# Optimization experiments

Hardware: AMD Instinct MI355X
Metric: run time of the kernel (lower is better)

## Reference

```python
import jax, jax.numpy as jnp
import numpy as np

B, RNN, WV, VOCAB, SRC, NMEM, OOV = 64, 512, 512, 50000, 512, 512, 50


def _gru_cell(x, h, wih, whh, bih, bhh):
    # PyTorch GRU cell. x,h: (B,RNN); wih,whh: (3*RNN, RNN)
    gi = x @ wih.T + bih
    gh = h @ whh.T + bhh
    i_r, i_z, i_n = jnp.split(gi, 3, axis=-1)
    h_r, h_z, h_n = jnp.split(gh, 3, axis=-1)
    r = jax.nn.sigmoid(i_r + h_r)
    z = jax.nn.sigmoid(i_z + h_z)
    n = jnp.tanh(i_n + r * h_n)
    return (1.0 - z) * n + z * h


def _attn_general(q, K, V, mask, W):
    # q: (B,1,D), K/V: (B,N,D), mask: (B,N), W: (D,D) (torch Linear weight, out x in)
    e = jnp.einsum('bnd,ed->bne', K, W)          # W(K)
    e = e * mask[:, :, None]
    en = jnp.einsum('btd,bnd->btn', q, e)        # (B,1,N)
    en = en * mask[:, None, :]
    # masked softmax: exp * mask, renormalize
    m = mask[:, None, :]
    ex = jnp.exp(en - jnp.max(en, axis=-1, keepdims=True)) * m
    w = ex / (jnp.sum(ex, axis=-1, keepdims=True) + 1e-10)
    ctx = jnp.einsum('btn,bnd->btd', w, V)       # (B,1,D)
    return ctx, w, en


def setup_inputs() -> dict:
    key = jax.random.key(0)
    ks = jax.random.split(key, 24)
    s = 0.05
    inp = {
        'y_t_1': jax.random.randint(ks[0], (B,), 0, VOCAB),
        's_t_1': jax.random.normal(ks[1], (1, B, RNN)) * s,
        'encoder_outputs': jax.random.normal(ks[2], (B, SRC, RNN)) * s,
        'enc_padding_mask': jnp.ones((B, SRC), jnp.float32),
        'c_t_1': jax.random.normal(ks[3], (B, 1, RNN)) * s,
        'extra_zeros': jnp.zeros((B, OOV), jnp.float32),
        'enc_batch_extend_vocab': jax.random.randint(ks[4], (B, SRC), 0, VOCAB + OOV),
        'query_memory': jax.random.normal(ks[5], (B, NMEM, RNN)) * s,
        'query_mask': jnp.ones((B, NMEM), jnp.float32),
        # parameters
        'embedding': jax.random.normal(ks[6], (VOCAB, WV)) * s,
        'x_ctx_w': jax.random.normal(ks[7], (RNN, RNN + WV)) * s,
        'x_ctx_b': jnp.zeros((RNN,), jnp.float32),
        'gru_wih': jax.random.uniform(ks[8], (3 * RNN, RNN), minval=-0.1, maxval=0.1),
        'gru_whh': jax.random.uniform(ks[9], (3 * RNN, RNN), minval=-0.1, maxval=0.1),
        'gru_bih': jnp.concatenate([jnp.zeros(RNN), jnp.ones(RNN // 2), jnp.zeros(3 * RNN - RNN - RNN // 2)]).astype(jnp.float32),
        'gru_bhh': jnp.zeros((3 * RNN,), jnp.float32),
        'readq_w': jax.random.normal(ks[10], (RNN, RNN)) * s,
        'readsrc_w': jax.random.normal(ks[11], (RNN, RNN)) * s,
        'out1_w': jax.random.normal(ks[12], (RNN, 2 * RNN)) * s,
        'out1_b': jnp.zeros((RNN,), jnp.float32),
        'out2_w': jax.random.normal(ks[13], (VOCAB, RNN)) * s,
        'out2_b': jnp.zeros((VOCAB,), jnp.float32),
    }
    return inp


def reference(y_t_1, s_t_1, encoder_outputs, enc_padding_mask, c_t_1, extra_zeros,
              enc_batch_extend_vocab, query_memory, query_mask,
              embedding, x_ctx_w, x_ctx_b, gru_wih, gru_whh, gru_bih, gru_bhh,
              readq_w, readsrc_w, out1_w, out1_b, out2_w, out2_b):
    # embed current token and mix with previous context
    y_emb = embedding[y_t_1]                                   # (B,WV)
    x = jnp.concatenate([c_t_1, y_emb[:, None, :]], axis=-1)   # (B,1,RNN+WV)
    x = x @ x_ctx_w.T + x_ctx_b                                # (B,1,RNN)

    h = s_t_1[0]                                               # (B,RNN)
    h = _gru_cell(x[:, 0], h, gru_wih, gru_whh, gru_bih, gru_bhh)

    # NTM memory read + second GRU step (loop runs once in the source)
    c_mem, _, _ = _attn_general(h[:, None, :], query_memory, query_memory, query_mask, readq_w)
    h = _gru_cell(c_mem[:, 0], h, gru_wih, gru_whh, gru_bih, gru_bhh)

    # source attention
    c_t, attn_dist, _ = _attn_general(h[:, None, :], encoder_outputs, encoder_outputs, enc_padding_mask, readsrc_w)

    out = jnp.concatenate([h, c_t[:, 0]], axis=-1)             # (B,2*RNN)
    out = out @ out1_w.T + out1_b
    out = out @ out2_w.T + out2_b                              # (B,VOCAB)
    vocab_dist = jax.nn.softmax(out, axis=-1)

    vocab_dist_ = 0.5 * vocab_dist
    attn_dist_ = 0.5 * attn_dist[:, 0]                         # (B,SRC)
    vocab_dist_ = jnp.concatenate([vocab_dist_, extra_zeros], axis=-1)  # (B,VOCAB+OOV)

    # copy-mechanism scatter_add along vocab dim, per batch row
    final_dist = jax.vmap(lambda v, idx, a: v.at[idx].add(a))(
        vocab_dist_, enc_batch_extend_vocab, attn_dist_)

    s_t = h[None]                                              # (1,B,RNN)
    return final_dist, s_t, c_t, attn_dist
```

## Files before the change

### kernel.cpp

```cpp
#include <hip/hip_runtime.h>

#define BATCH 64
#define RNN   512
#define VOCAB 50000
#define OOV   50
#define VEXT  50050
#define NSRC  512
#define NOB2  391

typedef short bf16x8 __attribute__((ext_vector_type(8)));
typedef float f32x4  __attribute__((ext_vector_type(4)));

__device__ __forceinline__ float sigmoidf_(float x) { return 1.f / (1.f + __expf(-x)); }

__device__ __forceinline__ float gru_one(float ir, float iz, float inn,
                                         float hr, float hz, float hn, float h)
{
    const float r = sigmoidf_(ir + hr);
    const float z = sigmoidf_(iz + hz);
    const float n = tanhf(inn + r * hn);
    return (1.f - z) * n + z * h;
}

__device__ __forceinline__ short f2bf(float x) {
    unsigned u = __builtin_bit_cast(unsigned, x);
    unsigned r = (u + 0x7FFFu + ((u >> 16) & 1u)) >> 16;
    return (short)r;
}

template<bool WT>
__global__ __launch_bounds__(256) void k_gemm_small(
    const float* __restrict__ A0, const float* __restrict__ W0,
    const float* __restrict__ bias0, float* __restrict__ C0, int asum0,
    const float* __restrict__ A1, const float* __restrict__ W1,
    const float* __restrict__ bias1, float* __restrict__ C1, int asum1,
    int K, int O)
{
    const float* A = A0; const float* W = W0; const float* bias = bias0;
    float* C = C0; int asum = asum0;
    if (blockIdx.z == 1) { A = A1; W = W1; bias = bias1; C = C1; asum = asum1; }

    __shared__ float As[32 * 64];
    __shared__ float Ws[32 * 32];
    const int t  = threadIdx.x;
    const int tx = t & 15, ty = t >> 4;
    const int o0 = blockIdx.x * 32;
    const int kchunk = K >> 2;
    const int kbeg = blockIdx.y * kchunk;
    const int kend = kbeg + kchunk;
    float acc[4][2] = {};
    const int ab  = t >> 2;
    const int akq = (t & 3) * 4;

    for (int k0 = kbeg; k0 < kend; k0 += 32) {
        {
            const float* Ap = &A[(size_t)ab * K + k0 + akq];
            float4 v0 = *(const float4*)Ap;
            float4 v1 = *(const float4*)(Ap + 16);
            if (asum) {
                #pragma unroll
                for (int s = 1; s < 4; s++) {
                    const float* Aps = Ap + (size_t)s * 64 * K;
                    float4 w0 = *(const float4*)Aps;
                    float4 w1 = *(const float4*)(Aps + 16);
                    v0.x += w0.x; v0.y += w0.y; v0.z += w0.z; v0.w += w0.w;
                    v1.x += w1.x; v1.y += w1.y; v1.z += w1.z; v1.w += w1.w;
                }
            }
            As[(akq+0)*64+ab]=v0.x; As[(akq+1)*64+ab]=v0.y; As[(akq+2)*64+ab]=v0.z; As[(akq+3)*64+ab]=v0.w;
            As[(akq+16)*64+ab]=v1.x; As[(akq+17)*64+ab]=v1.y; As[(akq+18)*64+ab]=v1.z; As[(akq+19)*64+ab]=v1.w;
        }
        if (WT) {
            const int o  = t >> 3;
            const int kq = (t & 7) * 4;
            float4 v = *(const float4*)&W[(size_t)(o0 + o) * K + k0 + kq];
            Ws[(kq+0)*32+o]=v.x; Ws[(kq+1)*32+o]=v.y; Ws[(kq+2)*32+o]=v.z; Ws[(kq+3)*32+o]=v.w;
        } else {
            const int kk = t >> 3;
            const int oq = (t & 7) * 4;
            *(float4*)&Ws[kk*32 + oq] = *(const float4*)&W[(size_t)(k0 + kk) * O + o0 + oq];
        }
        __syncthreads();
        #pragma unroll
        for (int kk = 0; kk < 32; kk++) {
            float4 a4 = *(const float4*)&As[kk*64 + ty*4];
            float2 w2 = *(const float2*)&Ws[kk*32 + tx*2];
            acc[0][0] = fmaf(a4.x, w2.x, acc[0][0]); acc[0][1] = fmaf(a4.x, w2.y, acc[0][1]);
            acc[1][0] = fmaf(a4.y, w2.x, acc[1][0]); acc[1][1] = fmaf(a4.y, w2.y, acc[1][1]);
            acc[2][0] = fmaf(a4.z, w2.x, acc[2][0]); acc[2][1] = fmaf(a4.z, w2.y, acc[2][1]);
            acc[3][0] = fmaf(a4.w, w2.x, acc[3][0]); acc[3][1] = fmaf(a4.w, w2.y, acc[3][1]);
        }
        __syncthreads();
    }
    const int o = o0 + tx*2;
    float b0v = 0.f, b1v = 0.f;
    if (bias && blockIdx.y == 0) { b0v = bias[o]; b1v = bias[o+1]; }
    float* Cp = C + (size_t)blockIdx.y * 64 * O;
    #pragma unroll
    for (int j = 0; j < 4; j++) {
        const int bb = ty*4 + j;
        Cp[(size_t)bb*O + o]     = acc[j][0] + b0v;
        Cp[(size_t)bb*O + o + 1] = acc[j][1] + b1v;
    }
}

__global__ __launch_bounds__(256) void k_gemm_x0(
    const int* __restrict__ yidx, const float* __restrict__ ct1, const float* __restrict__ emb,
    const float* __restrict__ W, const float* __restrict__ bias, float* __restrict__ C)
{
    __shared__ float As[32 * 64];
    __shared__ float Ws[32 * 32];
    const int t  = threadIdx.x;
    const int tx = t & 15, ty = t >> 4;
    const int o0 = blockIdx.x * 32;
    const int kbeg = blockIdx.y * 256;
    const int kend = kbeg + 256;
    float acc[4][2] = {};
    const int ab  = t >> 2;
    const int akq = (t & 3) * 4;
    const int erow = yidx[ab];

    for (int k0 = kbeg; k0 < kend; k0 += 32) {
        {
            const float* src = (k0 < 512) ? (ct1 + (size_t)ab * 512 + k0)
                                          : (emb + (size_t)erow * 512 + (k0 - 512));
            float4 v0 = *(const float4*)(src + akq);
            float4 v1 = *(const float4*)(src + akq + 16);
            As[(akq+0)*64+ab]=v0.x; As[(akq+1)*64+ab]=v0.y; As[(akq+2)*64+ab]=v0.z; As[(akq+3)*64+ab]=v0.w;
            As[(akq+16)*64+ab]=v1.x; As[(akq+17)*64+ab]=v1.y; As[(akq+18)*64+ab]=v1.z; As[(akq+19)*64+ab]=v1.w;
        }
        {
            const int o  = t >> 3;
            const int kq = (t & 7) * 4;
            float4 v = *(const float4*)&W[(size_t)(o0 + o) * 1024 + k0 + kq];
            Ws[(kq+0)*32+o]=v.x; Ws[(kq+1)*32+o]=v.y; Ws[(kq+2)*32+o]=v.z; Ws[(kq+3)*32+o]=v.w;
        }
        __syncthreads();
        #pragma unroll
        for (int kk = 0; kk < 32; kk++) {
            float4 a4 = *(const float4*)&As[kk*64 + ty*4];
            float2 w2 = *(const float2*)&Ws[kk*32 + tx*2];
            acc[0][0] = fmaf(a4.x, w2.x, acc[0][0]); acc[0][1] = fmaf(a4.x, w2.y, acc[0][1]);
            acc[1][0] = fmaf(a4.y, w2.x, acc[1][0]); acc[1][1] = fmaf(a4.y, w2.y, acc[1][1]);
            acc[2][0] = fmaf(a4.z, w2.x, acc[2][0]); acc[2][1] = fmaf(a4.z, w2.y, acc[2][1]);
            acc[3][0] = fmaf(a4.w, w2.x, acc[3][0]); acc[3][1] = fmaf(a4.w, w2.y, acc[3][1]);
        }
        __syncthreads();
    }
    const int o = o0 + tx*2;
    float b0v = 0.f, b1v = 0.f;
    if (blockIdx.y == 0) { b0v = bias[o]; b1v = bias[o+1]; }
    float* Cp = C + (size_t)blockIdx.y * 64 * 512;
    #pragma unroll
    for (int j = 0; j < 4; j++) {
        const int bb = ty*4 + j;
        Cp[(size_t)bb*512 + o]     = acc[j][0] + b0v;
        Cp[(size_t)bb*512 + o + 1] = acc[j][1] + b1v;
    }
}

template<int KS>
__global__ __launch_bounds__(256) void k_gemm_gru(
    const float* __restrict__ gi, const float* __restrict__ gh,
    const float* __restrict__ hprev, const float* __restrict__ W,
    float* __restrict__ C, float* __restrict__ hout, float* __restrict__ cat_out)
{
    __shared__ float As[32 * 64];
    __shared__ float Ws[32 * 32];
    const int t  = threadIdx.x;
    const int tx = t & 15, ty = t >> 4;
    const int o0 = blockIdx.x * 32;
    const int kchunk = 512 / KS;
    const int kbeg = blockIdx.y * kchunk;
    const int kend = kbeg + kchunk;
    float acc[4][2] = {};
    const int ab  = t >> 2;
    const int akq = (t & 3) * 4;

    for (int k0 = kbeg; k0 < kend; k0 += 32) {
        #pragma unroll
        for (int half = 0; half < 2; half++) {
            const int d = k0 + akq + half * 16;
            float irv[4] = {0,0,0,0}, izv[4] = {0,0,0,0}, inv_[4] = {0,0,0,0};
            float hrv[4] = {0,0,0,0}, hzv[4] = {0,0,0,0}, hnv[4] = {0,0,0,0};
            #pragma unroll
            for (int s = 0; s < 4; s++) {
                const float* gp = gi + (size_t)s * BATCH * 1536 + (size_t)ab * 1536 + d;
                const float* hp = gh + (size_t)s * BATCH * 1536 + (size_t)ab * 1536 + d;
                float4 a0 = *(const float4*)(gp);
                float4 a1 = *(const float4*)(gp + 512);
                float4 a2 = *(const float4*)(gp + 1024);
                float4 b0 = *(const float4*)(hp);
                float4 b1 = *(const float4*)(hp + 512);
                float4 b2 = *(const float4*)(hp + 1024);
                irv[0]+=a0.x; irv[1]+=a0.y; irv[2]+=a0.z; irv[3]+=a0.w;
                izv[0]+=a1.x; izv[1]+=a1.y; izv[2]+=a1.z; izv[3]+=a1.w;
                inv_[0]+=a2.x; inv_[1]+=a2.y; inv_[2]+=a2.z; inv_[3]+=a2.w;
                hrv[0]+=b0.x; hrv[1]+=b0.y; hrv[2]+=b0.z; hrv[3]+=b0.w;
                hzv[0]+=b1.x; hzv[1]+=b1.y; hzv[2]+=b1.z; hzv[3]+=b1.w;
                hnv[0]+=b2.x; hnv[1]+=b2.y; hnv[2]+=b2.z; hnv[3]+=b2.w;
            }
            const float4 hq = *(const float4*)(hprev + (size_t)ab * 512 + d);
            float o0v = gru_one(irv[0], izv[0], inv_[0], hrv[0], hzv[0], hnv[0], hq.x);
            float o1v = gru_one(irv[1], izv[1], inv_[1], hrv[1], hzv[1], hnv[1], hq.y);
            float o2v = gru_one(irv[2], izv[2], inv_[2], hrv[2], hzv[2], hnv[2], hq.z);
            float o3v = gru_one(irv[3], izv[3], inv_[3], hrv[3], hzv[3], hnv[3], hq.w);
            const int kk = akq + half * 16;
            As[(kk+0)*64+ab] = o0v; As[(kk+1)*64+ab] = o1v;
            As[(kk+2)*64+ab] = o2v; As[(kk+3)*64+ab] = o3v;
            if (blockIdx.x == 0) {
                float4 ov = make_float4(o0v, o1v, o2v, o3v);
                *(float4*)&hout[(size_t)ab * 512 + d] = ov;
                if (cat_out) *(float4*)&cat_out[(size_t)ab * 1024 + d] = ov;
            }
        }
        {
            const int kk = t >> 3;
            const int oq = (t & 7) * 4;
            *(float4*)&Ws[kk*32 + oq] = *(const float4*)&W[(size_t)(k0 + kk) * 512 + o0 + oq];
        }
        __syncthreads();
        #pragma unroll
        for (int kk = 0; kk < 32; kk++) {
            float4 a4 = *(const float4*)&As[kk*64 + ty*4];
            float2 w2 = *(const float2*)&Ws[kk*32 + tx*2];
            acc[0][0] = fmaf(a4.x, w2.x, acc[0][0]); acc[0][1] = fmaf(a4.x, w2.y, acc[0][1]);
            acc[1][0] = fmaf(a4.y, w2.x, acc[1][0]); acc[1][1] = fmaf(a4.y, w2.y, acc[1][1]);
            acc[2][0] = fmaf(a4.z, w2.x, acc[2][0]); acc[2][1] = fmaf(a4.z, w2.y, acc[2][1]);
            acc[3][0] = fmaf(a4.w, w2.x, acc[3][0]); acc[3][1] = fmaf(a4.w, w2.y, acc[3][1]);
        }
        __syncthreads();
    }
    const int o = o0 + tx*2;
    float* Cp = C + (size_t)blockIdx.y * 64 * 512;
    #pragma unroll
    for (int j = 0; j < 4; j++) {
        const int bb = ty*4 + j;
        Cp[(size_t)bb*512 + o]     = acc[j][0];
        Cp[(size_t)bb*512 + o + 1] = acc[j][1];
    }
}

__global__ __launch_bounds__(256) void k_attn_pass(
    const float* __restrict__ KV, const float* __restrict__ Upart,
    const float* __restrict__ mask, float* __restrict__ en, float* __restrict__ part)
{
    const int b = blockIdx.y;
    const int chunk = blockIdx.x;
    const int t = threadIdx.x;
    const int lane = t & 63;
    const int wv = t >> 6;
    const float* KVb = KV + (size_t)b * NSRC * RNN;

    const int r0 = chunk * 32 + wv * 8;

    float4 x[8][2];
    float mk[8];
    #pragma unroll
    for (int i = 0; i < 8; i++) {
        const float* rp = KVb + (size_t)(r0 + i) * RNN + lane * 8;
        x[i][0] = *(const float4*)rp;
        x[i][1] = *(const float4*)(rp + 4);
    }
    #pragma unroll
    for (int i = 0; i < 8; i++) mk[i] = mask[(size_t)b * NSRC + r0 + i];

    float4 u0, u1;
    {
        const float* up = Upart + (size_t)b * RNN + lane * 8;
        u0 = *(const float4*)up; u1 = *(const float4*)(up + 4);
        #pragma unroll
        for (int s = 1; s < 8; s++) {
            const float* ups = up + (size_t)s * BATCH * RNN;
            float4 a = *(const float4*)ups; float4 c = *(const float4*)(ups + 4);
            u0.x += a.x; u0.y += a.y; u0.z += a.z; u0.w += a.w;
            u1.x += c.x; u1.y += c.y; u1.z += c.z; u1.w += c.w;
        }
    }

    float m_run = -1e30f, s_run = 0.f;
    float acc[8] = {0,0,0,0,0,0,0,0};
    #pragma unroll
    for (int i = 0; i < 8; i++) {
        const int n = r0 + i;
        float d = x[i][0].x*u0.x + x[i][0].y*u0.y + x[i][0].z*u0.z + x[i][0].w*u0.w
                + x[i][1].x*u1.x + x[i][1].y*u1.y + x[i][1].z*u1.z + x[i][1].w*u1.w;
        #pragma unroll
        for (int off = 32; off; off >>= 1) d += __shfl_xor(d, off);
        const float s = d * mk[i] * mk[i];
        if (lane == 0) en[(size_t)b * NSRC + n] = s;
        const float mnew = fmaxf(m_run, s);
        const float sc = __expf(m_run - mnew);
        const float w  = __expf(s - mnew) * mk[i];
        s_run = s_run * sc + w;
        acc[0] = acc[0]*sc + w*x[i][0].x; acc[1] = acc[1]*sc + w*x[i][0].y;
        acc[2] = acc[2]*sc + w*x[i][0].z; acc[3] = acc[3]*sc + w*x[i][0].w;
        acc[4] = acc[4]*sc + w*x[i][1].x; acc[5] = acc[5]*sc + w*x[i][1].y;
        acc[6] = acc[6]*sc + w*x[i][1].z; acc[7] = acc[7]*sc + w*x[i][1].w;
        m_run = mnew;
    }
    __shared__ float sm[4], ss[4];
    __shared__ float sacc[4][512];
    *(float4*)&sacc[wv][lane*8]     = make_float4(acc[0], acc[1], acc[2], acc[3]);
    *(float4*)&sacc[wv][lane*8 + 4] = make_float4(acc[4], acc[5], acc[6], acc[7]);
    if (lane == 0) { sm[wv] = m_run; ss[wv] = s_run; }
    __syncthreads();
    const float M = fmaxf(fmaxf(sm[0], sm[1]), fmaxf(sm[2], sm[3]));
    const float e0 = __expf(sm[0]-M), e1 = __expf(sm[1]-M), e2 = __expf(sm[2]-M), e3 = __expf(sm[3]-M);
    const float S = ss[0]*e0 + ss[1]*e1 + ss[2]*e2 + ss[3]*e3;
    float* pp = part + (size_t)(b * 16 + chunk) * 514;
    const int c = t;
    pp[2 + c]       = sacc[0][c]*e0 + sacc[1][c]*e1 + sacc[2][c]*e2 + sacc[3][c]*e3;
    pp[2 + c + 256] = sacc[0][c+256]*e0 + sacc[1][c+256]*e1 + sacc[2][c+256]*e2 + sacc[3][c+256]*e3;
    if (t == 0) { pp[0] = M; pp[1] = S; }
}

__global__ __launch_bounds__(128) void k_attn_combine(
    const float* __restrict__ part, const float* __restrict__ en,
    const float* __restrict__ mask, float* __restrict__ ctx,
    float* __restrict__ ctx2, float* __restrict__ attn_out)
{
    const int b = blockIdx.x, z = blockIdx.y, t = threadIdx.x;
    const float* pb = part + (size_t)b * 16 * 514;
    float M = -1e30f;
    #pragma unroll
    for (int c = 0; c < 16; c++) M = fmaxf(M, pb[c * 514]);
    float e[16]; float S = 0.f;
    #pragma unroll
    for (int c = 0; c < 16; c++) { e[c] = __expf(pb[c * 514] - M); S += pb[c * 514 + 1] * e[c]; }
    const float inv = 1.f / (S + 1e-10f);
    const int d = z * 128 + t;
    float a = 0.f;
    #pragma unroll
    for (int c = 0; c < 16; c++) a += pb[c * 514 + 2 + d] * e[c];
    const float val = a * inv;
    ctx[(size_t)b * 512 + d] = val;
    if (ctx2) ctx2[(size_t)b * 1024 + d] = val;
    if (attn_out)
        attn_out[(size_t)b * NSRC + d] = __expf(en[(size_t)b * NSRC + d] - M) * mask[(size_t)b * NSRC + d] * inv;
}

__global__ void k_tobf16(const float* __restrict__ in, short* __restrict__ outp)
{
    const int i = blockIdx.x * 256 + threadIdx.x;
    const float v = in[i] + in[32768 + i] + in[65536 + i] + in[98304 + i];
    outp[i] = f2bf(v);
}

__global__ __launch_bounds__(512, 4) void k_out2_mfma(
    const short* __restrict__ Abf, const float* __restrict__ W2,
    const float* __restrict__ bias, float* __restrict__ C, float* __restrict__ bstat)
{
    __shared__ alignas(16) short As[64 * 512];
    __shared__ float smax[8][64];
    __shared__ float ssum[8][64];
    const int t = threadIdx.x;
    const int lane = t & 63, wv = t >> 6;

    {
        char* Asb = (char*)As;
        const char* Ab = (const char*)Abf;
        #pragma unroll
        for (int it = 0; it < 8; ++it) {
            const int off = (it * 512 + t) * 16;
            const int row = off >> 10;
            const int kb  = off & 1023;
            bf16x8 v = *(const bf16x8*)(Ab + off);
            *(bf16x8*)(Asb + row * 1024 + (kb ^ ((row & 7) << 4))) = v;
        }
    }
    __syncthreads();

    const int l15 = lane & 15, g = lane >> 4;
    const int goff = g * 8;
    const int obase = blockIdx.x * 128 + wv * 16;
    const int ocol = obase + l15;
    const bool valid = (ocol < VOCAB);
    const int orow = valid ? ocol : (VOCAB - 1);
    const float* wr = &W2[(size_t)orow * RNN + goff];

    const int sw = (l15 & 7) << 4;
    const char* a0b = (const char*)As + (l15     ) * 1024;
    const char* a1b = (const char*)As + (l15 + 16) * 1024;
    const char* a2b = (const char*)As + (l15 + 32) * 1024;
    const char* a3b = (const char*)As + (l15 + 48) * 1024;

    f32x4 acc0 = {0,0,0,0}, acc1 = {0,0,0,0}, acc2 = {0,0,0,0}, acc3 = {0,0,0,0};

    float4 p0a = *(const float4*)(wr);
    float4 p0b = *(const float4*)(wr + 4);
    float4 p1a = *(const float4*)(wr + 32);
    float4 p1b = *(const float4*)(wr + 36);
    #pragma unroll 4
    for (int k0 = 0; k0 < RNN; k0 += 32) {
        const int kn = (k0 + 64) & 511;
        float4 n0 = *(const float4*)(wr + kn);
        float4 n1 = *(const float4*)(wr + kn + 4);
        const int kb = ((k0 + goff) * 2) ^ sw;
        bf16x8 a0 = *(const bf16x8*)(a0b + kb);
        bf16x8 a1 = *(const bf16x8*)(a1b + kb);
        bf16x8 a2 = *(const bf16x8*)(a2b + kb);
        bf16x8 a3 = *(const bf16x8*)(a3b + kb);
        bf16x8 bf;
        bf[0]=f2bf(p0a.x); bf[1]=f2bf(p0a.y); bf[2]=f2bf(p0a.z); bf[3]=f2bf(p0a.w);
        bf[4]=f2bf(p0b.x); bf[5]=f2bf(p0b.y); bf[6]=f2bf(p0b.z); bf[7]=f2bf(p0b.w);
        acc0 = __builtin_amdgcn_mfma_f32_16x16x32_bf16(a0, bf, acc0, 0, 0, 0);
        acc1 = __builtin_amdgcn_mfma_f32_16x16x32_bf16(a1, bf, acc1, 0, 0, 0);
        acc2 = __builtin_amdgcn_mfma_f32_16x16x32_bf16(a2, bf, acc2, 0, 0, 0);
        acc3 = __builtin_amdgcn_mfma_f32_16x16x32_bf16(a3, bf, acc3, 0, 0, 0);
        p0a = p1a; p0b = p1b; p1a = n0; p1b = n1;
    }

    const float bv = valid ? bias[ocol] : 0.f;
    float lv[4][4];
    #pragma unroll
    for (int r = 0; r < 4; r++) {
        lv[0][r] = valid ? acc0[r] + bv : -1e30f;
        lv[1][r] = valid ? acc1[r] + bv : -1e30f;
        lv[2][r] = valid ? acc2[r] + bv : -1e30f;
        lv[3][r] = valid ? acc3[r] + bv : -1e30f;
    }
    if (valid) {
        #pragma unroll
        for (int q = 0; q < 4; q++)
            #pragma unroll
            for (int r = 0; r < 4; r++)
                C[(size_t)(q*16 + g*4 + r) * VOCAB + ocol] = lv[q][r];
    }

    #pragma unroll
    for (int q = 0; q < 4; q++) {
        #pragma unroll
        for (int r = 0; r < 4; r++) {
            float m = lv[q][r];
            m = fmaxf(m, __shfl_xor(m, 1));
            m = fmaxf(m, __shfl_xor(m, 2));
            m = fmaxf(m, __shfl_xor(m, 4));
            m = fmaxf(m, __shfl_xor(m, 8));
            if (l15 == 0) smax[wv][q*16 + g*4 + r] = m;
        }
    }
    __syncthreads();
    if (t < 64) {
        float m = smax[0][t];
        #pragma unroll
        for (int w = 1; w < 8; w++) m = fmaxf(m, smax[w][t]);
        smax[0][t] = m;
    }
    __syncthreads();
    #pragma unroll
    for (int q = 0; q < 4; q++) {
        #pragma unroll
        for (int r = 0; r < 4; r++) {
            const int row = q*16 + g*4 + r;
            float e = __expf(lv[q][r] - smax[0][row]);
            e += __shfl_xor(e, 1);
            e += __shfl_xor(e, 2);
            e += __shfl_xor(e, 4);
            e += __shfl_xor(e, 8);
            if (l15 == 0) ssum[wv][row] = e;
        }
    }
    __syncthreads();
    if (t < 64) {
        float s = 0.f;
        #pragma unroll
        for (int w = 0; w < 8; w++) s += ssum[w][t];
        bstat[((size_t)t * NOB2 + blockIdx.x) * 2 + 0] = smax[0][t];
        bstat[((size_t)t * NOB2 + blockIdx.x) * 2 + 1] = s;
    }
}

__global__ __launch_bounds__(256) void k_statred(const float* __restrict__ bstat, float* __restrict__ stat)
{
    const int b = blockIdx.x, t = threadIdx.x;
    const float* pr = bstat + (size_t)b * NOB2 * 2;
    __shared__ float red[8];
    float m = -1e30f;
    for (int i = t; i < NOB2; i += 256) m = fmaxf(m, pr[i*2]);
    #pragma unroll
    for (int off = 32; off; off >>= 1) m = fmaxf(m, __shfl_xor(m, off));
    if ((t & 63) == 0) red[t >> 6] = m;
    __syncthreads();
    m = fmaxf(fmaxf(red[0], red[1]), fmaxf(red[2], red[3]));
    __syncthreads();
    float s = 0.f;
    for (int i = t; i < NOB2; i += 256) s += pr[i*2+1] * __expf(pr[i*2] - m);
    #pragma unroll
    for (int off = 32; off; off >>= 1) s += __shfl_xor(s, off);
    if ((t & 63) == 0) red[(t >> 6) + 4] = s;
    __syncthreads();
    if (t == 0) { stat[b*2] = m; stat[b*2+1] = red[4]+red[5]+red[6]+red[7]; }
}

__global__ void k_final(const float* __restrict__ L, const float* __restrict__ stat,
                        const float* __restrict__ ez, float* __restrict__ out)
{
    const int b = blockIdx.y;
    const int v = blockIdx.x * 256 + threadIdx.x;
    if (v >= VEXT) return;
    const float M = stat[b * 2];
    const float inv = 0.5f / stat[b * 2 + 1];
    float r;
    if (v < VOCAB) r = __expf(L[(size_t)b * VOCAB + v] - M) * inv;
    else           r = ez[(size_t)b * OOV + (v - VOCAB)];
    out[(size_t)b * VEXT + v] = r;
}

__global__ void k_scatter(const int* __restrict__ idx, const float* __restrict__ attn,
                          float* __restrict__ out)
{
    const int b = blockIdx.x, j = threadIdx.x;
    const int v = idx[(size_t)b * NSRC + j];
    atomicAdd(&out[(size_t)b * VEXT + v], 0.5f * attn[(size_t)b * NSRC + j]);
}

extern "C" void kernel_launch(void* const* d_in, const int* in_sizes, int n_in,
                              void* d_out, int out_size, void* d_ws, size_t ws_size,
                              hipStream_t stream)
{
    (void)in_sizes; (void)n_in; (void)out_size; (void)ws_size;
    const int*   y     = (const int*)  d_in[0];
    const float* st1   = (const float*)d_in[1];
    const float* enc   = (const float*)d_in[2];
    const float* encM  = (const float*)d_in[3];
    const float* ct1   = (const float*)d_in[4];
    const float* ez    = (const float*)d_in[5];
    const int*   ebev  = (const int*)  d_in[6];
    const float* qmem  = (const float*)d_in[7];
    const float* qmask = (const float*)d_in[8];
    const float* emb   = (const float*)d_in[9];
    const float* xw    = (const float*)d_in[10];
    const float* xb    = (const float*)d_in[11];
    const float* wih   = (const float*)d_in[12];
    const float* whh   = (const float*)d_in[13];
    const float* bih   = (const float*)d_in[14];
    const float* bhh   = (const float*)d_in[15];
    const float* rqw   = (const float*)d_in[16];
    const float* rsw   = (const float*)d_in[17];
    const float* o1w   = (const float*)d_in[18];
    const float* o1b   = (const float*)d_in[19];
    const float* o2w   = (const float*)d_in[20];
    const float* o2b   = (const float*)d_in[21];

    float* ws  = (float*)d_ws;
    float* out = (float*)d_out;

    constexpr size_t WS_PART = 0;
    constexpr size_t WS_EN   = 526336;
    constexpr size_t WS_H1   = 559104;
    constexpr size_t WS_CTX1 = 591872;
    constexpr size_t WS_LOG  = 0;
    constexpr size_t WS_GIP  = 3200000;
    constexpr size_t WS_GHP  = 3593216;
    constexpr size_t WS_UP   = 3986432;
    constexpr size_t WS_XP   = 3986432;
    constexpr size_t WS_O1P  = 3986432;
    constexpr size_t WS_ABF  = 4117504;
    constexpr size_t WS_CAT2 = 4248576;
    constexpr size_t WS_BSTAT= 4314112;
    constexpr size_t WS_STAT = 4364160;

    constexpr size_t OUT_ST = 3203200, OUT_CT = 3235968, OUT_ATTN = 3268736;

    float* part = ws + WS_PART;
    float* en   = ws + WS_EN;
    float* h1   = ws + WS_H1;
    float* ctx1 = ws + WS_CTX1;
    float* logi = ws + WS_LOG;
    float* gip  = ws + WS_GIP;
    float* ghp  = ws + WS_GHP;
    float* up   = ws + WS_UP;
    float* xp   = ws + WS_XP;
    float* o1p  = ws + WS_O1P;
    float* cat2 = ws + WS_CAT2;
    float* bstat= ws + WS_BSTAT;
    float* stat = ws + WS_STAT;
    short* abf  = (short*)(ws + WS_ABF);

    k_gemm_x0<<<dim3(16,4), 256, 0, stream>>>(y, ct1, emb, xw, xb, xp);
    k_gemm_small<true><<<dim3(48,4,2), 256, 0, stream>>>(xp, wih, bih, gip, 1,
                                                         st1, whh, bhh, ghp, 0, 512, 1536);
    k_gemm_gru<8><<<dim3(16,8), 256, 0, stream>>>(gip, ghp, st1, rqw, up, h1, nullptr);
    k_attn_pass<<<dim3(16,64), 256, 0, stream>>>(qmem, up, qmask, en, part);
    k_attn_combine<<<dim3(64,4), 128, 0, stream>>>(part, en, qmask, ctx1, nullptr, nullptr);
    k_gemm_small<true><<<dim3(48,4,2), 256, 0, stream>>>(ctx1, wih, bih, gip, 0,
                                                         h1, whh, bhh, ghp, 0, 512, 1536);
    k_gemm_gru<8><<<dim3(16,8), 256, 0, stream>>>(gip, ghp, h1, rsw, up, out + OUT_ST, cat2);
    k_attn_pass<<<dim3(16,64), 256, 0, stream>>>(enc, up, encM, en, part);
    k_attn_combine<<<dim3(64,4), 128, 0, stream>>>(part, en, encM, out + OUT_CT, cat2 + 512, out + OUT_ATTN);
    k_gemm_small<true><<<dim3(16,4,1), 256, 0, stream>>>(cat2, o1w, o1b, o1p, 0,
                                                         nullptr, nullptr, nullptr, nullptr, 0, 1024, 512);
    k_tobf16<<<128, 256, 0, stream>>>(o1p, abf);
    k_out2_mfma<<<NOB2, 512, 0, stream>>>(abf, o2w, o2b, logi, bstat);
    k_statred<<<64, 256, 0, stream>>>(bstat, stat);
    k_final<<<dim3(196,64), 256, 0, stream>>>(logi, stat, ez, out);
    k_scatter<<<64, 512, 0, stream>>>(ebev, out + OUT_ATTN, out);
}
```

Measured before the change: 156.8 us.

## Fuse out1 GEMM with bf16 conversion and fold stat reduction into final softmax

Replaces the split-K out1 GEMM plus separate bf16 conversion kernel with one kernel. It does an in-block two-way K split, reduces through shared memory and writes bf16 directly. The per-row softmax statistic reduction is also folded into the final normalization kernel, with each thread now handling 8 outputs. This removes two launches and the intermediate partial-sum traffic. The cost is that every final block re-reduces the 391 per-block stats, and the out1 GEMM runs on only 16 blocks.

```diff
diff --git a/kernel.cpp b/kernel.cpp
--- a/kernel.cpp
+++ b/kernel.cpp
@@ -340,11 +340,66 @@
         attn_out[(size_t)b * NSRC + d] = __expf(en[(size_t)b * NSRC + d] - M) * mask[(size_t)b * NSRC + d] * inv;
 }
 
-__global__ void k_tobf16(const float* __restrict__ in, short* __restrict__ outp)
-{
-    const int i = blockIdx.x * 256 + threadIdx.x;
-    const float v = in[i] + in[32768 + i] + in[65536 + i] + in[98304 + i];
-    outp[i] = f2bf(v);
+__global__ __launch_bounds__(512) void k_gemm_o1bf(
+    const float* __restrict__ A, const float* __restrict__ W,
+    const float* __restrict__ bias, short* __restrict__ Cbf)
+{
+    __shared__ float As[2][32 * 64];
+    __shared__ float Ws[2][32 * 32];
+    __shared__ float Red[2048];
+    const int t  = threadIdx.x;
+    const int kh = t >> 8;
+    const int tl = t & 255;
+    const int tx = tl & 15, ty = tl >> 4;
+    const int o0 = blockIdx.x * 32;
+    const int ab = tl >> 2, akq = (tl & 3) * 4;
+    const int wo = tl >> 3, wq = (tl & 7) * 4;
+    const int kbeg = kh * 512, kend = kbeg + 512;
+    float acc[4][2] = {};
+
+    for (int k0 = kbeg; k0 < kend; k0 += 32) {
+        {
+            const float* Ap = &A[(size_t)ab * 1024 + k0 + akq];
+            float4 v0 = *(const float4*)Ap;
+            float4 v1 = *(const float4*)(Ap + 16);
+            As[kh][(akq+0)*64+ab]=v0.x; As[kh][(akq+1)*64+ab]=v0.y; As[kh][(akq+2)*64+ab]=v0.z; As[kh][(akq+3)*64+ab]=v0.w;
+            As[kh][(akq+16)*64+ab]=v1.x; As[kh][(akq+17)*64+ab]=v1.y; As[kh][(akq+18)*64+ab]=v1.z; As[kh][(akq+19)*64+ab]=v1.w;
+        }
+        {
+            float4 wv = *(const float4*)&W[(size_t)(o0 + wo) * 1024 + k0 + wq];
+            Ws[kh][(wq+0)*32+wo]=wv.x; Ws[kh][(wq+1)*32+wo]=wv.y; Ws[kh][(wq+2)*32+wo]=wv.z; Ws[kh][(wq+3)*32+wo]=wv.w;
+        }
+        __syncthreads();
+        #pragma unroll
+        for (int kk = 0; kk < 32; kk++) {
+            float4 a4 = *(const float4*)&As[kh][kk*64 + ty*4];
+            float2 w2 = *(const float2*)&Ws[kh][kk*32 + tx*2];
+            acc[0][0] = fmaf(a4.x, w2.x, acc[0][0]); acc[0][1] = fmaf(a4.x, w2.y, acc[0][1]);
+            acc[1][0] = fmaf(a4.y, w2.x, acc[1][0]); acc[1][1] = fmaf(a4.y, w2.y, acc[1][1]);
+            acc[2][0] = fmaf(a4.z, w2.x, acc[2][0]); acc[2][1] = fmaf(a4.z, w2.y, acc[2][1]);
+            acc[3][0] = fmaf(a4.w, w2.x, acc[3][0]); acc[3][1] = fmaf(a4.w, w2.y, acc[3][1]);
+        }
+        __syncthreads();
+    }
+    if (kh == 1) {
+        float* rp = &Red[tl * 8];
+        rp[0]=acc[0][0]; rp[1]=acc[0][1]; rp[2]=acc[1][0]; rp[3]=acc[1][1];
+        rp[4]=acc[2][0]; rp[5]=acc[2][1]; rp[6]=acc[3][0]; rp[7]=acc[3][1];
+    }
+    __syncthreads();
+    if (kh == 0) {
+        const float* rp = &Red[tl * 8];
+        const int o = o0 + tx*2;
+        const float b0 = bias[o], b1 = bias[o+1];
+        #pragma unroll
+        for (int j = 0; j < 4; j++) {
+            const int bb = ty*4 + j;
+            short2 s2;
+            s2.x = f2bf(acc[j][0] + rp[j*2+0] + b0);
+            s2.y = f2bf(acc[j][1] + rp[j*2+1] + b1);
+            *(short2*)&Cbf[(size_t)bb*512 + o] = s2;
+        }
+    }
 }
 
 __global__ __launch_bounds__(512, 4) void k_out2_mfma(
@@ -471,11 +526,13 @@
     }
 }
 
-__global__ __launch_bounds__(256) void k_statred(const float* __restrict__ bstat, float* __restrict__ stat)
-{
-    const int b = blockIdx.x, t = threadIdx.x;
+__global__ __launch_bounds__(256) void k_final(
+    const float* __restrict__ L, const float* __restrict__ bstat,
+    const float* __restrict__ ez, float* __restrict__ out)
+{
+    const int b = blockIdx.y, t = threadIdx.x;
     const float* pr = bstat + (size_t)b * NOB2 * 2;
-    __shared__ float red[8];
+    __shared__ float red[4];
     float m = -1e30f;
     for (int i = t; i < NOB2; i += 256) m = fmaxf(m, pr[i*2]);
     #pragma unroll
@@ -488,23 +545,37 @@
     for (int i = t; i < NOB2; i += 256) s += pr[i*2+1] * __expf(pr[i*2] - m);
     #pragma unroll
     for (int off = 32; off; off >>= 1) s += __shfl_xor(s, off);
-    if ((t & 63) == 0) red[(t >> 6) + 4] = s;
-    __syncthreads();
-    if (t == 0) { stat[b*2] = m; stat[b*2+1] = red[4]+red[5]+red[6]+red[7]; }
-}
-
-__global__ void k_final(const float* __restrict__ L, const float* __restrict__ stat,
-                        const float* __restrict__ ez, float* __restrict__ out)
-{
-    const int b = blockIdx.y;
-    const int v = blockIdx.x * 256 + threadIdx.x;
-    if (v >= VEXT) return;
-    const float M = stat[b * 2];
-    const float inv = 0.5f / stat[b * 2 + 1];
-    float r;
-    if (v < VOCAB) r = __expf(L[(size_t)b * VOCAB + v] - M) * inv;
-    else           r = ez[(size_t)b * OOV + (v - VOCAB)];
-    out[(size_t)b * VEXT + v] = r;
+    if ((t & 63) == 0) red[t >> 6] = s;
+    __syncthreads();
+    s = red[0] + red[1] + red[2] + red[3];
+    const float inv = 0.5f / s;
+
+    const int v0 = blockIdx.x * 2048 + t * 8;
+    if (v0 >= VEXT) return;
+    float* op = out + (size_t)b * VEXT + v0;
+    if (v0 + 8 <= VOCAB) {
+        const float* lp = L + (size_t)b * VOCAB + v0;
+        float4 x0 = *(const float4*)lp;
+        float4 x1 = *(const float4*)(lp + 4);
+        float2 r0 = make_float2(__expf(x0.x - m) * inv, __expf(x0.y - m) * inv);
+        float2 r1 = make_float2(__expf(x0.z - m) * inv, __expf(x0.w - m) * inv);
+        float2 r2 = make_float2(__expf(x1.x - m) * inv, __expf(x1.y - m) * inv);
+        float2 r3 = make_float2(__expf(x1.z - m) * inv, __expf(x1.w - m) * inv);
+        *(float2*)(op)     = r0;
+        *(float2*)(op + 2) = r1;
+        *(float2*)(op + 4) = r2;
+        *(float2*)(op + 6) = r3;
+    } else {
+        #pragma unroll
+        for (int e = 0; e < 8; e++) {
+            const int v = v0 + e;
+            if (v >= VEXT) break;
+            float r;
+            if (v < VOCAB) r = __expf(L[(size_t)b * VOCAB + v] - m) * inv;
+            else           r = ez[(size_t)b * OOV + (v - VOCAB)];
+            op[e] = r;
+        }
+    }
 }
 
 __global__ void k_scatter(const int* __restrict__ idx, const float* __restrict__ attn,
@@ -555,11 +626,9 @@
     constexpr size_t WS_GHP  = 3593216;
     constexpr size_t WS_UP   = 3986432;
     constexpr size_t WS_XP   = 3986432;
-    constexpr size_t WS_O1P  = 3986432;
     constexpr size_t WS_ABF  = 4117504;
     constexpr size_t WS_CAT2 = 4248576;
     constexpr size_t WS_BSTAT= 4314112;
-    constexpr size_t WS_STAT = 4364160;
 
     constexpr size_t OUT_ST = 3203200, OUT_CT = 3235968, OUT_ATTN = 3268736;
 
@@ -572,10 +641,8 @@
     float* ghp  = ws + WS_GHP;
     float* up   = ws + WS_UP;
     float* xp   = ws + WS_XP;
-    float* o1p  = ws + WS_O1P;
     float* cat2 = ws + WS_CAT2;
     float* bstat= ws + WS_BSTAT;
-    float* stat = ws + WS_STAT;
     short* abf  = (short*)(ws + WS_ABF);
 
     k_gemm_x0<<<dim3(16,4), 256, 0, stream>>>(y, ct1, emb, xw, xb, xp);
@@ -589,11 +656,8 @@
     k_gemm_gru<8><<<dim3(16,8), 256, 0, stream>>>(gip, ghp, h1, rsw, up, out + OUT_ST, cat2);
     k_attn_pass<<<dim3(16,64), 256, 0, stream>>>(enc, up, encM, en, part);
     k_attn_combine<<<dim3(64,4), 128, 0, stream>>>(part, en, encM, out + OUT_CT, cat2 + 512, out + OUT_ATTN);
-    k_gemm_small<true><<<dim3(16,4,1), 256, 0, stream>>>(cat2, o1w, o1b, o1p, 0,
-                                                         nullptr, nullptr, nullptr, nullptr, 0, 1024, 512);
-    k_tobf16<<<128, 256, 0, stream>>>(o1p, abf);
+    k_gemm_o1bf<<<16, 512, 0, stream>>>(cat2, o1w, o1b, abf);
     k_out2_mfma<<<NOB2, 512, 0, stream>>>(abf, o2w, o2b, logi, bstat);
-    k_statred<<<64, 256, 0, stream>>>(bstat, stat);
-    k_final<<<dim3(196,64), 256, 0, stream>>>(logi, stat, ez, out);
+    k_final<<<dim3(25,64), 256, 0, stream>>>(logi, bstat, ez, out);
     k_scatter<<<64, 512, 0, stream>>>(ebev, out + OUT_ATTN, out);
 }
```

Measured after the change: 173.2 us. 10.4% more time.
